# Kernel optimization log

Hardware: AMD Instinct MI355X
Metric: run time of the kernel (lower is better)

The kernel has to match this reference:

```python
import jax, jax.numpy as jnp
import numpy as np

E = 8      # num_experts
A = 128    # angle feature size = input_size - 4
TGT = 3    # target size
HID = 16   # expert MLP hidden / latent / main GRU hidden
OUT = 128  # motion decoder output size
B = 64
W = 128
F = A + TGT + 1  # 132
BN_EPS = 1e-5


def _gru_layer(x, Wih, Whh, bih, bhh):
    # x: (B, T, I); Wih: (3H, I); Whh: (3H, H). PyTorch GRU equations.
    xW = jnp.einsum('bti,gi->btg', x, Wih) + bih  # precompute input gates (B,T,3H)
    H = Whh.shape[1]

    def step(h, xw):
        gh = h @ Whh.T + bhh
        ir, iz, inn = jnp.split(xw, 3, axis=-1)
        hr, hz, hn = jnp.split(gh, 3, axis=-1)
        r = jax.nn.sigmoid(ir + hr)
        z = jax.nn.sigmoid(iz + hz)
        n = jnp.tanh(inn + r * hn)
        h_new = (1.0 - z) * n + z * h
        return h_new, h_new

    h0 = jnp.zeros((x.shape[0], H), x.dtype)
    _, ys = jax.lax.scan(step, h0, jnp.swapaxes(xW, 0, 1))
    return jnp.swapaxes(ys, 0, 1)  # (B, T, H)


def _expert_mlp(x, om, w1, b1, w2, b2, g, bt):
    # Blend expert weights per-sample, then matvec; fused as one einsum (same math).
    h = jnp.einsum('bi,be,eih->bh', x, om, w1) + om @ b1
    # BatchNorm1d, training-mode batch statistics (biased variance), then ELU
    m = h.mean(0)
    v = h.var(0)
    h = jax.nn.elu(g * (h - m) * jax.lax.rsqrt(v + BN_EPS) + bt)
    return jnp.einsum('bh,be,eho->bo', h, om, w2) + om @ b2


def _forward(Local, Remote,
             gW_ih0, gW_hh0, gb_ih0, gb_hh0, gW_ih1, gW_hh1, gb_ih1, gb_hh1,
             ae_w1, ae_b1, ae_w2, ae_b2, ae_g, ae_bt,
             md_w1, md_b1, md_w2, md_b2, md_g, md_bt,
             mW_ih0, mW_hh0, mb_ih0, mb_hh0, mW_ih1, mW_hh1, mb_ih1, mb_hh1):
    Bn, Wn, _ = Local.shape
    LA = Local[..., :A]
    RA = Remote[..., :A]
    LT = Local[..., A:A + TGT]
    RT = Remote[..., A:A + TGT]
    Scale = Remote[..., A + TGT]  # (B, W)

    def gate(t):
        h = _gru_layer(t, gW_ih0, gW_hh0, gb_ih0, gb_hh0)
        h = _gru_layer(h, gW_ih1, gW_hh1, gb_ih1, gb_hh1)
        return jax.nn.softmax(h, axis=-1)

    Lo = gate(LT)  # (B, W, E)
    Ro = gate(RT)

    ZL = _expert_mlp(LA.reshape(-1, A), Lo.reshape(-1, E), ae_w1, ae_b1, ae_w2, ae_b2, ae_g, ae_bt)
    ZR = _expert_mlp(RA.reshape(-1, A), Ro.reshape(-1, E), ae_w1, ae_b1, ae_w2, ae_b2, ae_g, ae_bt)
    Z = (ZL + ZR).reshape(Bn, Wn, HID)

    Z = _gru_layer(Z, mW_ih0, mW_hh0, mb_ih0, mb_hh0)
    Z = _gru_layer(Z, mW_ih1, mW_hh1, mb_ih1, mb_hh1)
    Z = Z[:, -1]  # (B, HID)

    dec_in = jnp.concatenate([Z, Scale[:, -1:]], axis=-1)  # (B, HID+1)
    return _expert_mlp(dec_in, Ro[:, -1], md_w1, md_b1, md_w2, md_b2, md_g, md_bt)


def setup_inputs() -> dict:
    key = jax.random.key(0)
    ks = iter(jax.random.split(key, 40))

    def u(shape, bound):
        return jax.random.uniform(next(ks), shape, jnp.float32, -bound, bound)

    d = {}
    d['Local'] = jax.random.normal(next(ks), (B, W, F), jnp.float32)
    d['Remote'] = jax.random.normal(next(ks), (B, W, F), jnp.float32)

    def gru_params(pref, isz, hsz):
        bd = 1.0 / np.sqrt(hsz)
        d[pref + 'W_ih0'] = u((3 * hsz, isz), bd)
        d[pref + 'W_hh0'] = u((3 * hsz, hsz), bd)
        d[pref + 'b_ih0'] = u((3 * hsz,), bd)
        d[pref + 'b_hh0'] = u((3 * hsz,), bd)
        d[pref + 'W_ih1'] = u((3 * hsz, hsz), bd)
        d[pref + 'W_hh1'] = u((3 * hsz, hsz), bd)
        d[pref + 'b_ih1'] = u((3 * hsz,), bd)
        d[pref + 'b_hh1'] = u((3 * hsz,), bd)

    gru_params('g', TGT, E)    # gating GRU: 2 layers, hidden = num_experts
    gru_params('m', HID, HID)  # main GRU: 2 layers, hidden = 16

    def expert(pref, isz, hsz, osz):
        b1 = float(np.sqrt(6.0 / (isz * hsz)))
        b2 = float(np.sqrt(6.0 / (hsz * osz)))
        d[pref + '_w1'] = u((E, isz, hsz), b1)
        d[pref + '_b1'] = jnp.zeros((E, hsz), jnp.float32)
        d[pref + '_w2'] = u((E, hsz, osz), b2)
        d[pref + '_b2'] = jnp.zeros((E, osz), jnp.float32)
        d[pref + '_g'] = jnp.ones((hsz,), jnp.float32)
        d[pref + '_bt'] = jnp.zeros((hsz,), jnp.float32)

    expert('ae', A, HID, HID)        # angle encoder
    expert('md', HID + 1, HID, OUT)  # motion decoder
    return d


def reference(Local, Remote,
              gW_ih0, gW_hh0, gb_ih0, gb_hh0, gW_ih1, gW_hh1, gb_ih1, gb_hh1,
              ae_w1, ae_b1, ae_w2, ae_b2, ae_g, ae_bt,
              md_w1, md_b1, md_w2, md_b2, md_g, md_bt,
              mW_ih0, mW_hh0, mb_ih0, mb_hh0, mW_ih1, mW_hh1, mb_ih1, mb_hh1):
    return _forward(Local, Remote,
                    gW_ih0, gW_hh0, gb_ih0, gb_hh0, gW_ih1, gW_hh1, gb_ih1, gb_hh1,
                    ae_w1, ae_b1, ae_w2, ae_b2, ae_g, ae_bt,
                    md_w1, md_b1, md_w2, md_b2, md_g, md_bt,
                    mW_ih0, mW_hh0, mb_ih0, mb_hh0, mW_ih1, mW_hh1, mb_ih1, mb_hh1)
```

## Files before the change

### kernel.cpp

```cpp
#include <hip/hip_runtime.h>
#include <cstdint>
#include <cstddef>

#define DEV __device__ __forceinline__

typedef float v2f __attribute__((ext_vector_type(2)));

DEV float fsig(float x)  { return __builtin_amdgcn_rcpf(1.0f + __expf(-x)); }
DEV float ftanh_(float x){ return 1.0f - 2.0f * __builtin_amdgcn_rcpf(1.0f + __expf(2.0f * x)); }
DEV float readlanef(float v, int l) {
    return __uint_as_float(__builtin_amdgcn_readlane(__float_as_uint(v), l));
}
DEV float bpermf(float v, int byteidx) {
    return __uint_as_float(__builtin_amdgcn_ds_bpermute(byteidx, __float_as_uint(v)));
}
DEV v2f fma2v(v2f a, float b, v2f c) {
    return (v2f){ fmaf(a.x, b, c.x), fmaf(a.y, b, c.y) };
}

constexpr size_t ACC   = 0;
constexpr size_t LO    = 128;
constexpr size_t RO    = LO + 65536;
constexpr size_t HBUF  = RO + 65536;
constexpr size_t XW0   = HBUF + 262144;
constexpr size_t ZLAST = XW0 + 393216;

__global__ __launch_bounds__(64) void k1_gate(
    const float* __restrict__ Local, const float* __restrict__ Remote,
    const float* __restrict__ Wih0, const float* __restrict__ Whh0,
    const float* __restrict__ bih0, const float* __restrict__ bhh0,
    const float* __restrict__ Wih1, const float* __restrict__ Whh1,
    const float* __restrict__ bih1, const float* __restrict__ bhh1,
    float* __restrict__ ws)
{
    const int tid = threadIdx.x;
    const int j = tid & 7;
    const int layer = (tid >> 3) & 1;
    const int blk = blockIdx.x;
    const int track = blk >> 6;
    const int b = blk & 63;
    if (blk == 0) ws[ACC + tid] = 0.f;

    __shared__ __align__(16) float4 xs4[128];
    __shared__ float h1all[128][9];

    const float* __restrict__ src = track ? Remote : Local;
    for (int t = tid; t < 128; t += 64) {
        const float* p = src + ((size_t)b * 128 + t) * 132 + 128;
        xs4[t] = make_float4(p[0], p[1], p[2], 0.f);
    }

    v2f wrz[19], wnn[19];
    float base_r, base_z, base_in, base_dn;
    if (layer == 0) {
#pragma unroll
        for (int k = 0; k < 8; ++k) {
            wrz[k] = (v2f){ Whh0[j * 8 + k], Whh0[(8 + j) * 8 + k] };
            wnn[k] = (v2f){ 0.f, Whh0[(16 + j) * 8 + k] };
            wrz[8 + k] = (v2f){0.f, 0.f};
            wnn[8 + k] = (v2f){0.f, 0.f};
        }
#pragma unroll
        for (int c = 0; c < 3; ++c) {
            wrz[16 + c] = (v2f){ Wih0[j * 3 + c], Wih0[(8 + j) * 3 + c] };
            wnn[16 + c] = (v2f){ Wih0[(16 + j) * 3 + c], 0.f };
        }
        base_r = bih0[j] + bhh0[j];
        base_z = bih0[8 + j] + bhh0[8 + j];
        base_in = bih0[16 + j];
        base_dn = bhh0[16 + j];
    } else {
#pragma unroll
        for (int k = 0; k < 8; ++k) {
            wrz[k] = (v2f){ Wih1[j * 8 + k], Wih1[(8 + j) * 8 + k] };
            wnn[k] = (v2f){ Wih1[(16 + j) * 8 + k], 0.f };
            wrz[8 + k] = (v2f){ Whh1[j * 8 + k], Whh1[(8 + j) * 8 + k] };
            wnn[8 + k] = (v2f){ 0.f, Whh1[(16 + j) * 8 + k] };
        }
#pragma unroll
        for (int c = 0; c < 3; ++c) {
            wrz[16 + c] = (v2f){0.f, 0.f};
            wnn[16 + c] = (v2f){0.f, 0.f};
        }
        base_r = bih1[j] + bhh1[j];
        base_z = bih1[8 + j] + bhh1[8 + j];
        base_in = bih1[16 + j];
        base_dn = bhh1[16 + j];
    }
    __syncthreads();

    float hown = 0.f;
    float4 xc = xs4[0];
#pragma unroll 1
    for (int t = 0; t <= 128; ++t) {
        float4 xn = xs4[t < 127 ? t + 1 : 127];
        float vb[16];
#pragma unroll
        for (int k = 0; k < 16; ++k) vb[k] = readlanef(hown, k);
        v2f arz = (v2f){ base_r, base_z };
        v2f ann = (v2f){ base_in, base_dn };
#pragma unroll
        for (int k = 0; k < 16; ++k) {
            arz = fma2v(wrz[k], vb[k], arz);
            ann = fma2v(wnn[k], vb[k], ann);
        }
        arz = fma2v(wrz[16], xc.x, arz); ann = fma2v(wnn[16], xc.x, ann);
        arz = fma2v(wrz[17], xc.y, arz); ann = fma2v(wnn[17], xc.y, ann);
        arz = fma2v(wrz[18], xc.z, arz); ann = fma2v(wnn[18], xc.z, ann);
        float r = fsig(arz.x);
        float z = fsig(arz.y);
        float n = ftanh_(ann.x + r * ann.y);
        float hnew = (1.f - z) * n + z * hown;
        bool act = layer ? (t >= 1) : (t < 128);
        hown = act ? hnew : hown;
        if (tid >= 8 && tid < 16 && t >= 1) h1all[t - 1][j] = hown;
        xc = xn;
    }
    __syncthreads();

    float* __restrict__ outp = ws + (track ? RO : LO);
    for (int t = tid; t < 128; t += 64) {
        float vv[8];
#pragma unroll
        for (int k = 0; k < 8; ++k) vv[k] = h1all[t][k];
        float mx = vv[0];
#pragma unroll
        for (int k = 1; k < 8; ++k) mx = fmaxf(mx, vv[k]);
        float ssum = 0.f;
#pragma unroll
        for (int k = 0; k < 8; ++k) { vv[k] = __expf(vv[k] - mx); ssum += vv[k]; }
        float inv = __builtin_amdgcn_rcpf(ssum);
        size_t base = ((size_t)b * 128 + t) * 8;
        float4 o0 = make_float4(vv[0] * inv, vv[1] * inv, vv[2] * inv, vv[3] * inv);
        float4 o1 = make_float4(vv[4] * inv, vv[5] * inv, vv[6] * inv, vv[7] * inv);
        *(float4*)(outp + base) = o0;
        *(float4*)(outp + base + 4) = o1;
    }
}

__global__ __launch_bounds__(256) void k2_expert1(
    const float* __restrict__ Local, const float* __restrict__ Remote,
    const float* __restrict__ ae_w1, const float* __restrict__ ae_b1,
    float* __restrict__ ws)
{
    const int blk = blockIdx.x;
    const int track = blk >> 7;
    const int n0 = (blk & 127) * 64;
    const float* __restrict__ X = track ? Remote : Local;
    const float* __restrict__ om = ws + (track ? RO : LO);

    __shared__ __align__(16) float xsh[64][64];
    __shared__ __align__(16) float wsh[16 * 516];
    __shared__ float omsh[64][8];
    __shared__ float b1sh[128];
    __shared__ float red[32];
    const int tid = threadIdx.x;

    for (int i = tid; i < 512; i += 256) omsh[i >> 3][i & 7] = om[(size_t)(n0 + (i >> 3)) * 8 + (i & 7)];
    for (int i = tid; i < 128; i += 256) b1sh[i] = ae_b1[i];
    if (tid < 32) red[tid] = 0.f;

    const int hh = tid & 15, rg = tid >> 4;
    float acc[4][8];
#pragma unroll
    for (int r = 0; r < 4; ++r)
#pragma unroll
        for (int e = 0; e < 8; ++e) acc[r][e] = 0.f;

    for (int kb = 0; kb < 2; ++kb) {
        __syncthreads();
        for (int i = tid; i < 4096; i += 256) {
            int r = i >> 6, k = i & 63;
            xsh[r][k] = X[(size_t)(n0 + r) * 132 + kb * 64 + k];
        }
        for (int i = tid; i < 8192; i += 256) {
            int h = i >> 9, e = (i >> 6) & 7, k = i & 63;
            wsh[h * 516 + e * 64 + k] = ae_w1[((size_t)e * 128 + kb * 64 + k) * 16 + h];
        }
        __syncthreads();
#pragma unroll 4
        for (int kq = 0; kq < 16; ++kq) {
            float4 xv[4], wv[8];
#pragma unroll
            for (int r = 0; r < 4; ++r) xv[r] = *(const float4*)&xsh[rg * 4 + r][kq * 4];
#pragma unroll
            for (int e = 0; e < 8; ++e) wv[e] = *(const float4*)&wsh[hh * 516 + e * 64 + kq * 4];
#pragma unroll
            for (int r = 0; r < 4; ++r)
#pragma unroll
                for (int e = 0; e < 8; ++e) {
                    float a = acc[r][e];
                    a = fmaf(xv[r].x, wv[e].x, a);
                    a = fmaf(xv[r].y, wv[e].y, a);
                    a = fmaf(xv[r].z, wv[e].z, a);
                    a = fmaf(xv[r].w, wv[e].w, a);
                    acc[r][e] = a;
                }
        }
    }

    float s = 0.f, s2 = 0.f;
    float* __restrict__ hout = ws + HBUF + (size_t)track * 131072;
#pragma unroll
    for (int r = 0; r < 4; ++r) {
        int row = rg * 4 + r;
        float hv = 0.f;
#pragma unroll
        for (int e = 0; e < 8; ++e) hv = fmaf(omsh[row][e], acc[r][e] + b1sh[e * 16 + hh], hv);
        hout[(size_t)(n0 + row) * 16 + hh] = hv;
        s += hv; s2 += hv * hv;
    }
    __syncthreads();
    atomicAdd(&red[hh], s);
    atomicAdd(&red[16 + hh], s2);
    __syncthreads();
    if (tid < 32) atomicAdd(&ws[ACC + track * 32 + tid], red[tid]);
}

__global__ __launch_bounds__(256) void k3_bn_mlp2(
    const float* __restrict__ ae_w2, const float* __restrict__ ae_b2,
    const float* __restrict__ ae_g, const float* __restrict__ ae_bt,
    const float* __restrict__ mWih0, const float* __restrict__ mbih0,
    float* __restrict__ ws)
{
    const int n0 = blockIdx.x * 64;
    const int tid = threadIdx.x;
    __shared__ float actsh[2][64][16];
    __shared__ float omsh[2][64][8];
    __shared__ float w2sh[2048];
    __shared__ float b2sh[128];
    __shared__ float zsh[64][17];
    __shared__ float wihsh[48][17];
    __shared__ float bihsh[48];
    __shared__ float stat[4][16];

    if (tid < 32) {
        int trk = tid >> 4, h = tid & 15;
        float s = ws[ACC + trk * 32 + h], s2 = ws[ACC + trk * 32 + 16 + h];
        float m = s * (1.f / 8192.f);
        float v = fmaxf(s2 * (1.f / 8192.f) - m * m, 0.f);
        stat[trk * 2][h] = m;
        stat[trk * 2 + 1][h] = rsqrtf(v + 1e-5f);
    }
    for (int i = tid; i < 2048; i += 256) w2sh[i] = ae_w2[i];
    for (int i = tid; i < 128; i += 256) b2sh[i] = ae_b2[i];
    for (int i = tid; i < 768; i += 256) wihsh[i >> 4][i & 15] = mWih0[i];
    if (tid < 48) bihsh[tid] = mbih0[tid];
    for (int i = tid; i < 1024; i += 256) {
        int trk = i >> 9, r = (i >> 3) & 63, e = i & 7;
        omsh[trk][r][e] = ws[(trk ? RO : LO) + (size_t)(n0 + r) * 8 + e];
    }
    __syncthreads();

    for (int i = tid; i < 2048; i += 256) {
        int trk = i >> 10, r = (i >> 4) & 63, h = i & 15;
        float v = ws[HBUF + (size_t)trk * 131072 + (size_t)(n0 + r) * 16 + h];
        float a = ae_g[h] * (v - stat[trk * 2][h]) * stat[trk * 2 + 1][h] + ae_bt[h];
        actsh[trk][r][h] = a > 0.f ? a : expm1f(a);
    }
    __syncthreads();

    for (int i = tid; i < 1024; i += 256) {
        int r = i >> 4, o = i & 15;
        float accv = 0.f;
#pragma unroll
        for (int trk = 0; trk < 2; ++trk) {
#pragma unroll
            for (int e = 0; e < 8; ++e) {
                const float* w = &w2sh[e * 256 + o];
                float t = b2sh[e * 16 + o];
#pragma unroll
                for (int h = 0; h < 16; ++h) t = fmaf(actsh[trk][r][h], w[h * 16], t);
                accv = fmaf(omsh[trk][r][e], t, accv);
            }
        }
        zsh[r][o] = accv;
    }
    __syncthreads();

    for (int i = tid; i < 3072; i += 256) {
        int r = i / 48, gr = i - r * 48;
        float a = bihsh[gr];
#pragma unroll
        for (int k = 0; k < 16; ++k) a = fmaf(zsh[r][k], wihsh[gr][k], a);
        ws[XW0 + (size_t)(n0 + r) * 48 + gr] = a;
    }
}

__global__ __launch_bounds__(64) void k4_maingru(
    const float* __restrict__ Whh0, const float* __restrict__ bhh0,
    const float* __restrict__ Wih1, const float* __restrict__ Whh1,
    const float* __restrict__ bih1, const float* __restrict__ bhh1,
    float* __restrict__ ws)
{
    const int tid = threadIdx.x;
    const int j = tid & 15;
    const int layer = (tid >> 4) & 1;
    const int half = tid >> 5;
    const int seq = blockIdx.x;

    __shared__ __align__(16) float4 xw4[1536];
    float* xwsh = (float*)xw4;

    const float4* __restrict__ xsrc = (const float4*)(ws + XW0 + (size_t)seq * 6144);
    for (int i = tid; i < 1536; i += 64) xw4[i] = xsrc[i];

    v2f wrz[16], wnn[16];
    float base_r, base_z, base_in, base_dn;
    if (layer == 0) {
        if (half == 0) {
#pragma unroll
            for (int k = 0; k < 16; ++k) {
                wrz[k] = (v2f){ Whh0[j * 16 + k], Whh0[(16 + j) * 16 + k] };
                wnn[k] = (v2f){ 0.f, Whh0[(32 + j) * 16 + k] };
            }
        } else {
#pragma unroll
            for (int k = 0; k < 16; ++k) { wrz[k] = (v2f){0.f,0.f}; wnn[k] = (v2f){0.f,0.f}; }
        }
        base_r = half ? 0.f : bhh0[j];
        base_z = half ? 0.f : bhh0[16 + j];
        base_in = 0.f;
        base_dn = half ? 0.f : bhh0[32 + j];
    } else {
        if (half == 0) {
#pragma unroll
            for (int k = 0; k < 16; ++k) {
                wrz[k] = (v2f){ Wih1[j * 16 + k], Wih1[(16 + j) * 16 + k] };
                wnn[k] = (v2f){ Wih1[(32 + j) * 16 + k], 0.f };
            }
        } else {
#pragma unroll
            for (int k = 0; k < 16; ++k) {
                wrz[k] = (v2f){ Whh1[j * 16 + k], Whh1[(16 + j) * 16 + k] };
                wnn[k] = (v2f){ 0.f, Whh1[(32 + j) * 16 + k] };
            }
        }
        base_r = half ? 0.f : (bih1[j] + bhh1[j]);
        base_z = half ? 0.f : (bih1[16 + j] + bhh1[16 + j]);
        base_in = half ? 0.f : bih1[32 + j];
        base_dn = half ? 0.f : bhh1[32 + j];
    }
    const float m0f = (layer == 0 && half == 0) ? 1.f : 0.f;
    const int ibase = half << 6;
    const int lid = __builtin_amdgcn_mbcnt_hi(~0u, __builtin_amdgcn_mbcnt_lo(~0u, 0u));
    const int pidx = (lid ^ 32) << 2;
    __syncthreads();

    float hown = 0.f;
    float p0 = xwsh[j], p1 = xwsh[16 + j], p2 = xwsh[32 + j];
#pragma unroll 1
    for (int t = 0; t <= 128; ++t) {
        int tn = (t < 127 ? t + 1 : 127) * 48;
        float q0 = xwsh[tn + j], q1 = xwsh[tn + 16 + j], q2 = xwsh[tn + 32 + j];
        float vb[16];
#pragma unroll
        for (int k = 0; k < 16; ++k) vb[k] = bpermf(hown, ibase + 4 * k);
        v2f arz = (v2f){ fmaf(m0f, p0, base_r), fmaf(m0f, p1, base_z) };
        v2f ann = (v2f){ fmaf(m0f, p2, base_in), base_dn };
#pragma unroll
        for (int k = 0; k < 16; ++k) {
            arz = fma2v(wrz[k], vb[k], arz);
            ann = fma2v(wnn[k], vb[k], ann);
        }
        float sr = arz.x + bpermf(arz.x, pidx);
        float sz = arz.y + bpermf(arz.y, pidx);
        float si = ann.x + bpermf(ann.x, pidx);
        float sd = ann.y + bpermf(ann.y, pidx);
        float r = fsig(sr);
        float z = fsig(sz);
        float n = ftanh_(si + r * sd);
        float hnew = (1.f - z) * n + z * hown;
        bool act = layer ? (t >= 1) : (t < 128);
        hown = act ? hnew : hown;
        p0 = q0; p1 = q1; p2 = q2;
    }
    if (tid >= 16 && tid < 32) ws[ZLAST + (size_t)seq * 16 + j] = hown;
}

__global__ __launch_bounds__(256) void k5_dec(
    const float* __restrict__ Remote,
    const float* __restrict__ md_w1, const float* __restrict__ md_b1,
    const float* __restrict__ md_g, const float* __restrict__ md_bt,
    const float* __restrict__ md_w2, const float* __restrict__ md_b2,
    const float* __restrict__ ws, float* __restrict__ out)
{
    const int o0 = blockIdx.x * 8;
    const int tid = threadIdx.x;
    __shared__ float xsh[64][17];
    __shared__ float omsh[64][8];
    __shared__ float w1sh[2176];
    __shared__ float b1sh[128];
    __shared__ float hsh[64][17];
    __shared__ float ssum[16], ss2[16], mstat[2][16];
    __shared__ float ash[64][17];
    __shared__ float w2sh[8][16][8];
    __shared__ float b2sh[8][8];

    for (int i = tid; i < 1024; i += 256) xsh[i >> 4][i & 15] = ws[ZLAST + i];
    if (tid < 64) xsh[tid][16] = Remote[((size_t)tid * 128 + 127) * 132 + 131];
    for (int i = tid; i < 512; i += 256)
        omsh[i >> 3][i & 7] = ws[RO + ((size_t)(i >> 3) * 128 + 127) * 8 + (i & 7)];
    for (int i = tid; i < 2176; i += 256) w1sh[i] = md_w1[i];
    for (int i = tid; i < 128; i += 256) b1sh[i] = md_b1[i];
    for (int i = tid; i < 1024; i += 256) {
        int e = i >> 7, h = (i >> 3) & 15, oo = i & 7;
        w2sh[e][h][oo] = md_w2[((size_t)e * 16 + h) * 128 + o0 + oo];
    }
    if (tid < 64) b2sh[tid >> 3][tid & 7] = md_b2[(size_t)(tid >> 3) * 128 + o0 + (tid & 7)];
    if (tid < 16) { ssum[tid] = 0.f; ss2[tid] = 0.f; }
    __syncthreads();

    for (int i = tid; i < 1024; i += 256) {
        int b = i >> 4, h = i & 15;
        float accv = 0.f;
#pragma unroll
        for (int e = 0; e < 8; ++e) {
            float t = b1sh[e * 16 + h];
            const float* w = &w1sh[e * 272 + h];
#pragma unroll
            for (int i2 = 0; i2 < 17; ++i2) t = fmaf(xsh[b][i2], w[i2 * 16], t);
            accv = fmaf(omsh[b][e], t, accv);
        }
        hsh[b][h] = accv;
        atomicAdd(&ssum[h], accv);
        atomicAdd(&ss2[h], accv * accv);
    }
    __syncthreads();
    if (tid < 16) {
        float m = ssum[tid] * (1.f / 64.f);
        float v = fmaxf(ss2[tid] * (1.f / 64.f) - m * m, 0.f);
        mstat[0][tid] = m;
        mstat[1][tid] = rsqrtf(v + 1e-5f);
    }
    __syncthreads();
    for (int i = tid; i < 1024; i += 256) {
        int b = i >> 4, h = i & 15;
        float a = md_g[h] * (hsh[b][h] - mstat[0][h]) * mstat[1][h] + md_bt[h];
        ash[b][h] = a > 0.f ? a : expm1f(a);
    }
    __syncthreads();

    for (int i = tid; i < 512; i += 256) {
        int b = i >> 3, oo = i & 7;
        float accv = 0.f;
#pragma unroll
        for (int e = 0; e < 8; ++e) {
            float t = b2sh[e][oo];
#pragma unroll
            for (int h = 0; h < 16; ++h) t = fmaf(ash[b][h], w2sh[e][h][oo], t);
            accv = fmaf(omsh[b][e], t, accv);
        }
        out[(size_t)b * 128 + o0 + oo] = accv;
    }
}

extern "C" void kernel_launch(void* const* d_in, const int* in_sizes, int n_in,
                              void* d_out, int out_size, void* d_ws, size_t ws_size,
                              hipStream_t stream) {
    const float* Local  = (const float*)d_in[0];
    const float* Remote = (const float*)d_in[1];
    const float* gWih0  = (const float*)d_in[2];
    const float* gWhh0  = (const float*)d_in[3];
    const float* gbih0  = (const float*)d_in[4];
    const float* gbhh0  = (const float*)d_in[5];
    const float* gWih1  = (const float*)d_in[6];
    const float* gWhh1  = (const float*)d_in[7];
    const float* gbih1  = (const float*)d_in[8];
    const float* gbhh1  = (const float*)d_in[9];
    const float* mWih0  = (const float*)d_in[10];
    const float* mWhh0  = (const float*)d_in[11];
    const float* mbih0  = (const float*)d_in[12];
    const float* mbhh0  = (const float*)d_in[13];
    const float* mWih1  = (const float*)d_in[14];
    const float* mWhh1  = (const float*)d_in[15];
    const float* mbih1  = (const float*)d_in[16];
    const float* mbhh1  = (const float*)d_in[17];
    const float* ae_w1  = (const float*)d_in[18];
    const float* ae_b1  = (const float*)d_in[19];
    const float* ae_w2  = (const float*)d_in[20];
    const float* ae_b2  = (const float*)d_in[21];
    const float* ae_g   = (const float*)d_in[22];
    const float* ae_bt  = (const float*)d_in[23];
    const float* md_w1  = (const float*)d_in[24];
    const float* md_b1  = (const float*)d_in[25];
    const float* md_w2  = (const float*)d_in[26];
    const float* md_b2  = (const float*)d_in[27];
    const float* md_g   = (const float*)d_in[28];
    const float* md_bt  = (const float*)d_in[29];
    float* ws  = (float*)d_ws;
    float* out = (float*)d_out;

    k1_gate<<<128, 64, 0, stream>>>(Local, Remote, gWih0, gWhh0, gbih0, gbhh0,
                                    gWih1, gWhh1, gbih1, gbhh1, ws);
    k2_expert1<<<256, 256, 0, stream>>>(Local, Remote, ae_w1, ae_b1, ws);
    k3_bn_mlp2<<<128, 256, 0, stream>>>(ae_w2, ae_b2, ae_g, ae_bt, mWih0, mbih0, ws);
    k4_maingru<<<64, 64, 0, stream>>>(mWhh0, mbhh0, mWih1, mWhh1, mbih1, mbhh1, ws);
    k5_dec<<<16, 256, 0, stream>>>(Remote, md_w1, md_b1, md_g, md_bt,
                                   md_w2, md_b2, ws, out);
}
```

Before: 254.5 us.

## Precompute gate input projections, load full expert tile once, use readlane in main GRU

In the gate GRU kernel, the layer-0 input projection (3 inputs times 24 gates plus bias) is computed into shared memory before the recurrence, removing three FMA pairs per step from the serial loop. The first expert kernel now stages the full 128-wide input rows and all expert weights in shared memory in one pass, dropping the two-phase K loop and its extra barriers at the cost of more LDS. The main GRU kernel no longer splits each matvec across two half-waves with bpermute exchanges; each lane does the full 32-term dot product using scalar readlane broadcasts, which shortens the per-step dependency chain but doubles the per-lane FMAs and register weights.

```diff
diff --git a/kernel.cpp b/kernel.cpp
--- a/kernel.cpp
+++ b/kernel.cpp
@@ -10,9 +10,6 @@
 DEV float ftanh_(float x){ return 1.0f - 2.0f * __builtin_amdgcn_rcpf(1.0f + __expf(2.0f * x)); }
 DEV float readlanef(float v, int l) {
     return __uint_as_float(__builtin_amdgcn_readlane(__float_as_uint(v), l));
-}
-DEV float bpermf(float v, int byteidx) {
-    return __uint_as_float(__builtin_amdgcn_ds_bpermute(byteidx, __float_as_uint(v)));
 }
 DEV v2f fma2v(v2f a, float b, v2f c) {
     return (v2f){ fmaf(a.x, b, c.x), fmaf(a.y, b, c.y) };
@@ -41,16 +38,24 @@
     const int b = blk & 63;
     if (blk == 0) ws[ACC + tid] = 0.f;
 
-    __shared__ __align__(16) float4 xs4[128];
+    __shared__ float xwg[128][24];
     __shared__ float h1all[128][9];
 
     const float* __restrict__ src = track ? Remote : Local;
     for (int t = tid; t < 128; t += 64) {
         const float* p = src + ((size_t)b * 128 + t) * 132 + 128;
-        xs4[t] = make_float4(p[0], p[1], p[2], 0.f);
-    }
-
-    v2f wrz[19], wnn[19];
+        float x0 = p[0], x1 = p[1], x2 = p[2];
+#pragma unroll
+        for (int u = 0; u < 24; ++u) {
+            float a = bih0[u];
+            a = fmaf(Wih0[u * 3 + 0], x0, a);
+            a = fmaf(Wih0[u * 3 + 1], x1, a);
+            a = fmaf(Wih0[u * 3 + 2], x2, a);
+            xwg[t][u] = a;
+        }
+    }
+
+    v2f wrz[16], wnn[16];
     float base_r, base_z, base_in, base_dn;
     if (layer == 0) {
 #pragma unroll
@@ -60,14 +65,9 @@
             wrz[8 + k] = (v2f){0.f, 0.f};
             wnn[8 + k] = (v2f){0.f, 0.f};
         }
-#pragma unroll
-        for (int c = 0; c < 3; ++c) {
-            wrz[16 + c] = (v2f){ Wih0[j * 3 + c], Wih0[(8 + j) * 3 + c] };
-            wnn[16 + c] = (v2f){ Wih0[(16 + j) * 3 + c], 0.f };
-        }
-        base_r = bih0[j] + bhh0[j];
-        base_z = bih0[8 + j] + bhh0[8 + j];
-        base_in = bih0[16 + j];
+        base_r = bhh0[j];
+        base_z = bhh0[8 + j];
+        base_in = 0.f;
         base_dn = bhh0[16 + j];
     } else {
 #pragma unroll
@@ -77,36 +77,30 @@
             wrz[8 + k] = (v2f){ Whh1[j * 8 + k], Whh1[(8 + j) * 8 + k] };
             wnn[8 + k] = (v2f){ 0.f, Whh1[(16 + j) * 8 + k] };
         }
-#pragma unroll
-        for (int c = 0; c < 3; ++c) {
-            wrz[16 + c] = (v2f){0.f, 0.f};
-            wnn[16 + c] = (v2f){0.f, 0.f};
-        }
         base_r = bih1[j] + bhh1[j];
         base_z = bih1[8 + j] + bhh1[8 + j];
         base_in = bih1[16 + j];
         base_dn = bhh1[16 + j];
     }
+    const float m0f = (layer == 0) ? 1.f : 0.f;
     __syncthreads();
 
     float hown = 0.f;
-    float4 xc = xs4[0];
+    float p0 = xwg[0][j], p1 = xwg[0][8 + j], p2 = xwg[0][16 + j];
 #pragma unroll 1
     for (int t = 0; t <= 128; ++t) {
-        float4 xn = xs4[t < 127 ? t + 1 : 127];
+        int tn = t < 127 ? t + 1 : 127;
+        float q0 = xwg[tn][j], q1 = xwg[tn][8 + j], q2 = xwg[tn][16 + j];
         float vb[16];
 #pragma unroll
         for (int k = 0; k < 16; ++k) vb[k] = readlanef(hown, k);
-        v2f arz = (v2f){ base_r, base_z };
-        v2f ann = (v2f){ base_in, base_dn };
+        v2f arz = (v2f){ fmaf(m0f, p0, base_r), fmaf(m0f, p1, base_z) };
+        v2f ann = (v2f){ fmaf(m0f, p2, base_in), base_dn };
 #pragma unroll
         for (int k = 0; k < 16; ++k) {
             arz = fma2v(wrz[k], vb[k], arz);
             ann = fma2v(wnn[k], vb[k], ann);
         }
-        arz = fma2v(wrz[16], xc.x, arz); ann = fma2v(wnn[16], xc.x, ann);
-        arz = fma2v(wrz[17], xc.y, arz); ann = fma2v(wnn[17], xc.y, ann);
-        arz = fma2v(wrz[18], xc.z, arz); ann = fma2v(wnn[18], xc.z, ann);
         float r = fsig(arz.x);
         float z = fsig(arz.y);
         float n = ftanh_(ann.x + r * ann.y);
@@ -114,7 +108,7 @@
         bool act = layer ? (t >= 1) : (t < 128);
         hown = act ? hnew : hown;
         if (tid >= 8 && tid < 16 && t >= 1) h1all[t - 1][j] = hown;
-        xc = xn;
+        p0 = q0; p1 = q1; p2 = q2;
     }
     __syncthreads();
 
@@ -149,16 +143,32 @@
     const float* __restrict__ X = track ? Remote : Local;
     const float* __restrict__ om = ws + (track ? RO : LO);
 
-    __shared__ __align__(16) float xsh[64][64];
-    __shared__ __align__(16) float wsh[16 * 516];
+    __shared__ __align__(16) float xsh[64 * 132];
+    __shared__ __align__(16) float wsh[16 * 1040];
     __shared__ float omsh[64][8];
     __shared__ float b1sh[128];
     __shared__ float red[32];
     const int tid = threadIdx.x;
 
+    for (int i = tid; i < 2048; i += 256) {
+        int r = i >> 5, q = i & 31;
+        ((float4*)&xsh[r * 132])[q] = ((const float4*)(X + (size_t)(n0 + r) * 132))[q];
+    }
+    for (int i4 = tid; i4 < 4096; i4 += 256) {
+        float4 v = ((const float4*)ae_w1)[i4];
+        int i = i4 * 4;
+#pragma unroll
+        for (int c = 0; c < 4; ++c) {
+            int ii = i + c;
+            int h = ii & 15, kk = (ii >> 4) & 127, e = ii >> 11;
+            float vc = c == 0 ? v.x : c == 1 ? v.y : c == 2 ? v.z : v.w;
+            wsh[h * 1040 + e * 130 + kk] = vc;
+        }
+    }
     for (int i = tid; i < 512; i += 256) omsh[i >> 3][i & 7] = om[(size_t)(n0 + (i >> 3)) * 8 + (i & 7)];
     for (int i = tid; i < 128; i += 256) b1sh[i] = ae_b1[i];
     if (tid < 32) red[tid] = 0.f;
+    __syncthreads();
 
     const int hh = tid & 15, rg = tid >> 4;
     float acc[4][8];
@@ -167,36 +177,24 @@
 #pragma unroll
         for (int e = 0; e < 8; ++e) acc[r][e] = 0.f;
 
-    for (int kb = 0; kb < 2; ++kb) {
-        __syncthreads();
-        for (int i = tid; i < 4096; i += 256) {
-            int r = i >> 6, k = i & 63;
-            xsh[r][k] = X[(size_t)(n0 + r) * 132 + kb * 64 + k];
-        }
-        for (int i = tid; i < 8192; i += 256) {
-            int h = i >> 9, e = (i >> 6) & 7, k = i & 63;
-            wsh[h * 516 + e * 64 + k] = ae_w1[((size_t)e * 128 + kb * 64 + k) * 16 + h];
-        }
-        __syncthreads();
 #pragma unroll 4
-        for (int kq = 0; kq < 16; ++kq) {
-            float4 xv[4], wv[8];
-#pragma unroll
-            for (int r = 0; r < 4; ++r) xv[r] = *(const float4*)&xsh[rg * 4 + r][kq * 4];
-#pragma unroll
-            for (int e = 0; e < 8; ++e) wv[e] = *(const float4*)&wsh[hh * 516 + e * 64 + kq * 4];
-#pragma unroll
-            for (int r = 0; r < 4; ++r)
-#pragma unroll
-                for (int e = 0; e < 8; ++e) {
-                    float a = acc[r][e];
-                    a = fmaf(xv[r].x, wv[e].x, a);
-                    a = fmaf(xv[r].y, wv[e].y, a);
-                    a = fmaf(xv[r].z, wv[e].z, a);
-                    a = fmaf(xv[r].w, wv[e].w, a);
-                    acc[r][e] = a;
-                }
-        }
+    for (int kq = 0; kq < 32; ++kq) {
+        float4 xv[4], wv[8];
+#pragma unroll
+        for (int r = 0; r < 4; ++r) xv[r] = *(const float4*)&xsh[(rg * 4 + r) * 132 + kq * 4];
+#pragma unroll
+        for (int e = 0; e < 8; ++e) wv[e] = *(const float4*)&wsh[hh * 1040 + e * 130 + kq * 4];
+#pragma unroll
+        for (int r = 0; r < 4; ++r)
+#pragma unroll
+            for (int e = 0; e < 8; ++e) {
+                float a = acc[r][e];
+                a = fmaf(xv[r].x, wv[e].x, a);
+                a = fmaf(xv[r].y, wv[e].y, a);
+                a = fmaf(xv[r].z, wv[e].z, a);
+                a = fmaf(xv[r].w, wv[e].w, a);
+                acc[r][e] = a;
+            }
     }
 
     float s = 0.f, s2 = 0.f;
@@ -296,7 +294,6 @@
     const int tid = threadIdx.x;
     const int j = tid & 15;
     const int layer = (tid >> 4) & 1;
-    const int half = tid >> 5;
     const int seq = blockIdx.x;
 
     __shared__ __align__(16) float4 xw4[1536];
@@ -305,46 +302,34 @@
     const float4* __restrict__ xsrc = (const float4*)(ws + XW0 + (size_t)seq * 6144);
     for (int i = tid; i < 1536; i += 64) xw4[i] = xsrc[i];
 
-    v2f wrz[16], wnn[16];
+    v2f wrz[32], wnn[32];
     float base_r, base_z, base_in, base_dn;
     if (layer == 0) {
-        if (half == 0) {
-#pragma unroll
-            for (int k = 0; k < 16; ++k) {
-                wrz[k] = (v2f){ Whh0[j * 16 + k], Whh0[(16 + j) * 16 + k] };
-                wnn[k] = (v2f){ 0.f, Whh0[(32 + j) * 16 + k] };
-            }
-        } else {
-#pragma unroll
-            for (int k = 0; k < 16; ++k) { wrz[k] = (v2f){0.f,0.f}; wnn[k] = (v2f){0.f,0.f}; }
-        }
-        base_r = half ? 0.f : bhh0[j];
-        base_z = half ? 0.f : bhh0[16 + j];
+#pragma unroll
+        for (int k = 0; k < 16; ++k) {
+            wrz[k] = (v2f){ Whh0[j * 16 + k], Whh0[(16 + j) * 16 + k] };
+            wnn[k] = (v2f){ 0.f, Whh0[(32 + j) * 16 + k] };
+            wrz[16 + k] = (v2f){0.f, 0.f};
+            wnn[16 + k] = (v2f){0.f, 0.f};
+        }
+        base_r = bhh0[j];
+        base_z = bhh0[16 + j];
         base_in = 0.f;
-        base_dn = half ? 0.f : bhh0[32 + j];
+        base_dn = bhh0[32 + j];
     } else {
-        if (half == 0) {
-#pragma unroll
-            for (int k = 0; k < 16; ++k) {
-                wrz[k] = (v2f){ Wih1[j * 16 + k], Wih1[(16 + j) * 16 + k] };
-                wnn[k] = (v2f){ Wih1[(32 + j) * 16 + k], 0.f };
-            }
-        } else {
-#pragma unroll
-            for (int k = 0; k < 16; ++k) {
-                wrz[k] = (v2f){ Whh1[j * 16 + k], Whh1[(16 + j) * 16 + k] };
-                wnn[k] = (v2f){ 0.f, Whh1[(32 + j) * 16 + k] };
-            }
-        }
-        base_r = half ? 0.f : (bih1[j] + bhh1[j]);
-        base_z = half ? 0.f : (bih1[16 + j] + bhh1[16 + j]);
-        base_in = half ? 0.f : bih1[32 + j];
-        base_dn = half ? 0.f : bhh1[32 + j];
-    }
-    const float m0f = (layer == 0 && half == 0) ? 1.f : 0.f;
-    const int ibase = half << 6;
-    const int lid = __builtin_amdgcn_mbcnt_hi(~0u, __builtin_amdgcn_mbcnt_lo(~0u, 0u));
-    const int pidx = (lid ^ 32) << 2;
+#pragma unroll
+        for (int k = 0; k < 16; ++k) {
+            wrz[k] = (v2f){ Wih1[j * 16 + k], Wih1[(16 + j) * 16 + k] };
+            wnn[k] = (v2f){ Wih1[(32 + j) * 16 + k], 0.f };
+            wrz[16 + k] = (v2f){ Whh1[j * 16 + k], Whh1[(16 + j) * 16 + k] };
+            wnn[16 + k] = (v2f){ 0.f, Whh1[(32 + j) * 16 + k] };
+        }
+        base_r = bih1[j] + bhh1[j];
+        base_z = bih1[16 + j] + bhh1[16 + j];
+        base_in = bih1[32 + j];
+        base_dn = bhh1[32 + j];
+    }
+    const float m0f = (layer == 0) ? 1.f : 0.f;
     __syncthreads();
 
     float hown = 0.f;
@@ -353,23 +338,19 @@
     for (int t = 0; t <= 128; ++t) {
         int tn = (t < 127 ? t + 1 : 127) * 48;
         float q0 = xwsh[tn + j], q1 = xwsh[tn + 16 + j], q2 = xwsh[tn + 32 + j];
-        float vb[16];
-#pragma unroll
-        for (int k = 0; k < 16; ++k) vb[k] = bpermf(hown, ibase + 4 * k);
+        float vb[32];
+#pragma unroll
+        for (int k = 0; k < 32; ++k) vb[k] = readlanef(hown, k);
         v2f arz = (v2f){ fmaf(m0f, p0, base_r), fmaf(m0f, p1, base_z) };
         v2f ann = (v2f){ fmaf(m0f, p2, base_in), base_dn };
 #pragma unroll
-        for (int k = 0; k < 16; ++k) {
+        for (int k = 0; k < 32; ++k) {
             arz = fma2v(wrz[k], vb[k], arz);
             ann = fma2v(wnn[k], vb[k], ann);
         }
-        float sr = arz.x + bpermf(arz.x, pidx);
-        float sz = arz.y + bpermf(arz.y, pidx);
-        float si = ann.x + bpermf(ann.x, pidx);
-        float sd = ann.y + bpermf(ann.y, pidx);
-        float r = fsig(sr);
-        float z = fsig(sz);
-        float n = ftanh_(si + r * sd);
+        float r = fsig(arz.x);
+        float z = fsig(arz.y);
+        float n = ftanh_(ann.x + r * ann.y);
         float hnew = (1.f - z) * n + z * hown;
         bool act = layer ? (t >= 1) : (t < 128);
         hown = act ? hnew : hown;
```

Result: slower. 264.9 us (+4.1%).
